# Kernel tuning notes

Measured on AMD Instinct MI355X. Metric: run time of the kernel, lower is better.

Reference implementation:

```python
import jax, jax.numpy as jnp
import numpy as np

N_E = 1024
E_DIM = 256
TAU = 0.5
BETA = 0.25
LAMB = 0.1
EPS = 1e-10


def setup_inputs() -> dict:
    key = jax.random.key(0)
    k1, k2, k3 = jax.random.split(key, 3)
    z = jax.random.normal(k1, (16, 1024, E_DIM), dtype=jnp.float32)
    # kaiming-normal-initialized codebook (std = sqrt(2 / fan_in))
    emb = jax.random.normal(k2, (N_E, E_DIM), dtype=jnp.float32) * np.sqrt(2.0 / E_DIM)
    u = jax.random.uniform(k3, (16 * 1024, N_E), dtype=jnp.float32)
    return {"z": z, "emb": emb, "u": u}


def reference(z, emb, u):
    zf = z.reshape(-1, E_DIM)                                  # [N, e_dim]
    # squared euclidean distances to each code: ||z||^2 + ||e||^2 - 2 z.e
    d = (jnp.sum(zf * zf, axis=1, keepdims=True)
         + jnp.sum(emb * emb, axis=1)
         - 2.0 * jnp.matmul(zf, emb.T))                        # [N, n_e]
    # gumbel-softmax (hard, straight-through) on logits = -d
    g = -jnp.log(-jnp.log(u + EPS) + EPS)
    y_soft = jax.nn.softmax((-d + g) / TAU, axis=-1)
    idx = jnp.argmax(y_soft, axis=-1)
    y_hard = jax.nn.one_hot(idx, N_E, dtype=y_soft.dtype)
    probs = y_hard + y_soft - jax.lax.stop_gradient(y_soft)    # [N, n_e]
    z_q = jnp.matmul(probs, emb).reshape(z.shape)
    # orthogonality loss on the codebook gram matrix
    gram = jnp.matmul(emb, emb.T)
    ortho = jnp.mean((gram - jnp.eye(N_E, dtype=emb.dtype)) ** 2) / (N_E ** 2)
    emb_loss = jnp.mean((jax.lax.stop_gradient(z_q) - z) ** 2)
    commit = BETA * jnp.mean((z_q - jax.lax.stop_gradient(z)) ** 2)
    loss = emb_loss + BETA * commit + LAMB * ortho
    z_q_st = z + jax.lax.stop_gradient(z_q - z)
    e_mean = jnp.mean(probs, axis=0)
    perplexity = jnp.exp(-jnp.sum(e_mean * jnp.log(e_mean + EPS)))
    return loss, z_q_st, perplexity
```

## Files before the change

kernel.cpp:

```cpp
#include <hip/hip_runtime.h>
#include <math.h>
#include <stdint.h>


#define NROWS 16384
#define NE    1024
#define ED    256
#define EPSF  1e-10f
#define INV2048 4.8828125e-4f
#define BM 128
#define BN 64
#define SCW 68

typedef _Float16 half_t;
typedef __attribute__((ext_vector_type(4))) _Float16 half4;
typedef __attribute__((ext_vector_type(8))) _Float16 half8;
typedef __attribute__((ext_vector_type(16))) float floatx16;
typedef unsigned long long u64;

__device__ __forceinline__ void gl_lds16(const void* g, void* l) {
    __builtin_amdgcn_global_load_lds(
        (const __attribute__((address_space(1))) uint32_t*)g,
        (__attribute__((address_space(3))) uint32_t*)l, 16, 0, 0);
}

__device__ __forceinline__ u64 packMax(float v, int code) {
    unsigned int b   = __float_as_uint(v);
    unsigned int key = (b & 0x80000000u) ? ~b : (b | 0x80000000u);
    return ((u64)key << 32) | (unsigned int)(NE - 1 - code);
}

__global__ __launch_bounds__(256) void vq_prep(
        const float* __restrict__ z, const float* __restrict__ emb,
        half_t* __restrict__ zh, half_t* __restrict__ zl,
        half_t* __restrict__ eh, half_t* __restrict__ el,
        float* __restrict__ enorm, float* __restrict__ znorm,
        u64* __restrict__ best)
{
    const int gid = blockIdx.x * 256 + threadIdx.x;
    const int ZQ4 = NROWS * ED / 4;
    if (gid < ZQ4) {
        const float4 v = ((const float4*)z)[gid];
        const float x[4] = {v.x, v.y, v.z, v.w};
        half4 h, l;
#pragma unroll
        for (int i = 0; i < 4; ++i) {
            const half_t hi = (half_t)x[i];
            h[i] = hi; l[i] = (half_t)((x[i] - (float)hi) * 2048.0f);
        }
        *(half4*)&zh[(size_t)gid * 4] = h;
        *(half4*)&zl[(size_t)gid * 4] = l;
        float s = v.x*v.x + v.y*v.y + v.z*v.z + v.w*v.w;
#pragma unroll
        for (int o = 32; o; o >>= 1) s += __shfl_down(s, o);
        if ((threadIdx.x & 63) == 0) znorm[gid >> 6] = s;
    } else {
        const int eg = gid - ZQ4;
        const float4 v = ((const float4*)emb)[eg];
        const float x[4] = {v.x, v.y, v.z, v.w};
        half4 h, l;
#pragma unroll
        for (int i = 0; i < 4; ++i) {
            const half_t hi = (half_t)x[i];
            h[i] = hi; l[i] = (half_t)((x[i] - (float)hi) * 2048.0f);
        }
        *(half4*)&eh[(size_t)eg * 4] = h;
        *(half4*)&el[(size_t)eg * 4] = l;
        float s = v.x*v.x + v.y*v.y + v.z*v.z + v.w*v.w;
#pragma unroll
        for (int o = 32; o; o >>= 1) s += __shfl_down(s, o);
        if ((threadIdx.x & 63) == 0) enorm[eg >> 6] = s;
        if (eg < NROWS) best[eg] = 0ull;
    }
}

__global__ __launch_bounds__(256, 2) void vq_gemm(
        const half_t* __restrict__ zh, const half_t* __restrict__ zl,
        const half_t* __restrict__ eh, const half_t* __restrict__ el,
        const float* __restrict__ u, const float* __restrict__ enorm,
        u64* __restrict__ best)
{
    __shared__ __align__(16) char smem[49152];
    half_t* SM = (half_t*)smem;
    float (*Sc)[SCW] = (float(*)[SCW])smem;
    u64* parr = (u64*)(smem + 34816);

    const int t    = threadIdx.x;
    const int w    = t >> 6;
    const int lane = t & 63;
    const int lrow = lane & 31;
    const int hw   = lane >> 5;

    const int bid = blockIdx.x;
    const int xcd = bid & 7, c = bid >> 3;
    const int m0 = (xcd * 16 + (c >> 4)) * BM;
    const int n0 = (c & 15) * BN;
    const int wm = (w >> 1) * 64, wn = (w & 1) * 32;

    size_t gaoff[2]; size_t gboff;
#pragma unroll
    for (int it = 0; it < 2; ++it) {
        const int s = it * 256 + t;
        const int row = s >> 2;
        const int cc = (s & 3) ^ ((row >> 1) & 3);
        gaoff[it] = (size_t)(m0 + row) * ED + cc * 8;
    }
    {
        const int row = t >> 2;
        const int cc = (t & 3) ^ ((row >> 1) & 3);
        gboff = (size_t)(n0 + row) * ED + cc * 8;
    }

    auto STAGE = [&](int kt, int b) {
        half_t* base = SM + b * 12288;
        const int kh = kt * 32;
#pragma unroll
        for (int it = 0; it < 2; ++it) {
            const int ldso = (it * 256 + w * 64) * 8;
            gl_lds16(zh + gaoff[it] + kh, base + ldso);
            gl_lds16(zl + gaoff[it] + kh, base + 4096 + ldso);
        }
        gl_lds16(eh + gboff + kh, base + 8192  + w * 64 * 8);
        gl_lds16(el + gboff + kh, base + 10240 + w * 64 * 8);
    };

    floatx16 accH[2] = {};
    floatx16 accX[2] = {};
    const int   col0 = n0 + wn + lrow;
    const float en0  = enorm[col0];
    float ur[2][16];

    STAGE(0, 0);
    __syncthreads();

#pragma unroll
    for (int kt = 0; kt < 8; ++kt) {
        const int cb = kt & 1;
        if (kt + 1 < 8) STAGE(kt + 1, cb ^ 1);
        if (kt == 0) {
            const float* ub = u + (size_t)(m0 + wm + (hw << 2)) * NE + col0;
#pragma unroll
            for (int i = 0; i < 2; ++i)
#pragma unroll
                for (int r = 0; r < 16; ++r)
                    ur[i][r] = ub[(size_t)(i * 32 + (r & 3) + ((r >> 2) << 3)) * NE];
        }
        {
            half_t* base = SM + cb * 12288;
#pragma unroll
            for (int ks = 0; ks < 2; ++ks) {
                const int cch = ks * 2 + hw;
                const int br = wn + lrow;
                const int sb = br * 4 + (cch ^ ((br >> 1) & 3));
                const half8 bh = *(const half8*)&base[8192  + sb * 8];
                const half8 bl = *(const half8*)&base[10240 + sb * 8];
                half8 ah[2], al[2];
#pragma unroll
                for (int i = 0; i < 2; ++i) {
                    const int ar = wm + i * 32 + lrow;
                    const int sa = ar * 4 + (cch ^ ((ar >> 1) & 3));
                    ah[i] = *(const half8*)&base[sa * 8];
                    al[i] = *(const half8*)&base[4096 + sa * 8];
                }
#pragma unroll
                for (int i = 0; i < 2; ++i) {
                    accH[i] = __builtin_amdgcn_mfma_f32_32x32x16_f16(ah[i], bh, accH[i], 0, 0, 0);
                    accX[i] = __builtin_amdgcn_mfma_f32_32x32x16_f16(ah[i], bl, accX[i], 0, 0, 0);
                    accX[i] = __builtin_amdgcn_mfma_f32_32x32x16_f16(al[i], bh, accX[i], 0, 0, 0);
                }
            }
        }
        if (kt == 0) {
#pragma unroll
            for (int i = 0; i < 2; ++i)
#pragma unroll
                for (int r = 0; r < 16; ++r)
                    asm volatile("" :: "v"(ur[i][r]));
        }
        __syncthreads();
    }

#pragma unroll
    for (int i = 0; i < 2; ++i) {
#pragma unroll
        for (int r = 0; r < 16; ++r) {
            const int lr = wm + i * 32 + (r & 3) + ((r >> 2) << 3) + (hw << 2);
            const float d = accH[i][r] + accX[i][r] * INV2048;
            const float g = -__logf(-__logf(ur[i][r] + EPSF) + EPSF);
            Sc[lr][wn + lrow] = 2.f * d - en0 + g;
        }
    }
    __syncthreads();

    {
        const int row = t >> 1;
        const int ch  = (t & 1) << 5;
        float bv = -1e38f; int bc = 0;
#pragma unroll
        for (int q = 0; q < 8; ++q) {
            const float4 v = *(const float4*)&Sc[row][ch + (q << 2)];
            const int cc = n0 + ch + (q << 2);
            if (v.x > bv) { bv = v.x; bc = cc; }
            if (v.y > bv) { bv = v.y; bc = cc + 1; }
            if (v.z > bv) { bv = v.z; bc = cc + 2; }
            if (v.w > bv) { bv = v.w; bc = cc + 3; }
        }
        parr[t] = packMax(bv, bc);
    }
    __syncthreads();
    if (t < 128) {
        const u64 a = parr[t << 1], b = parr[(t << 1) + 1];
        atomicMax(&best[m0 + t], a > b ? a : b);
    }
}

__global__ __launch_bounds__(256) void vq_outstore(
        const float* __restrict__ emb, const u64* __restrict__ best,
        float* __restrict__ out)
{
    __shared__ int ridx[8];
    const int t  = threadIdx.x;
    const int m0 = blockIdx.x * 8;

    if (t < 8)
        ridx[t] = NE - 1 - (int)(best[m0 + t] & 0xFFFFFFFFu);
    __syncthreads();

#pragma unroll
    for (int rr = 0; rr < 8; ++rr) {
        const int j = ridx[rr];
        out[1 + (size_t)(m0 + rr) * ED + t] = emb[(size_t)j * ED + t];
    }
}

__global__ __launch_bounds__(256) void vq_fin(
        const u64* __restrict__ best, const float* __restrict__ znorm,
        const float* __restrict__ u, float* __restrict__ out)
{
    __shared__ int    hist[NE];
    __shared__ double redl[4], redp[4];
    const int t = threadIdx.x;

    for (int i = t; i < NE; i += 256) hist[i] = 0;
    __syncthreads();

    double lsum = 0.0;
#pragma unroll 8
    for (int r = t; r < NROWS; r += 256) {
        const u64 p = best[r];
        const unsigned int key = (unsigned int)(p >> 32);
        const int code = NE - 1 - (int)(p & 0xFFFFFFFFu);
        atomicAdd(&hist[code], 1);
        const unsigned int b = (key & 0x80000000u) ? (key ^ 0x80000000u) : ~key;
        const float s  = __uint_as_float(b);
        const float uv = u[(size_t)r * NE + code];
        const float g  = -__logf(-__logf(uv + EPSF) + EPSF);
        lsum += (double)(znorm[r] - s + g);
    }
    __syncthreads();

    double psum = 0.0;
    for (int i = t; i < NE; i += 256) {
        const float em = (float)hist[i] / (float)NROWS;
        psum += (double)(em * logf(em + EPSF));
    }

#pragma unroll
    for (int o = 32; o; o >>= 1) { lsum += __shfl_down(lsum, o); psum += __shfl_down(psum, o); }
    if ((t & 63) == 0) { redl[t >> 6] = lsum; redp[t >> 6] = psum; }
    __syncthreads();
    if (t == 0) {
        const double mse = (redl[0] + redl[1] + redl[2] + redl[3])
                           / (double)((size_t)NROWS * ED);
        const double tot = redp[0] + redp[1] + redp[2] + redp[3];
        out[0] = (float)(mse * 1.0625);
        out[1 + (size_t)NROWS * ED] = (float)exp(-tot);
    }
}

extern "C" void kernel_launch(void* const* d_in, const int* in_sizes, int n_in,
                              void* d_out, int out_size, void* d_ws, size_t ws_size,
                              hipStream_t stream) {
    const float* z   = (const float*)d_in[0];
    const float* emb = (const float*)d_in[1];
    const float* u   = (const float*)d_in[2];
    float* out = (float*)d_out;

    float*  enorm    = (float*)((char*)d_ws + 5120);
    u64*    best     = (u64*)((char*)d_ws + 9216);
    float*  znorm    = (float*)((char*)d_ws + 140288);
    const size_t small_end = 205824;

    const size_t zsplit = (size_t)NROWS * ED * 2;
    const size_t esplit = (size_t)NE * ED * 2;
    const bool bigws = ws_size >= small_end + 2 * zsplit + 2 * esplit;

    half_t *zh, *zl, *eh, *el;
    if (bigws) {
        char* big = (char*)d_ws + small_end;
        zh = (half_t*)big;
        zl = (half_t*)(big + zsplit);
        eh = (half_t*)(big + 2 * zsplit);
        el = (half_t*)(big + 2 * zsplit + esplit);
    } else {
        zh = (half_t*)((char*)d_out + 8);
        zl = (half_t*)((char*)d_out + 8 + zsplit);
        eh = (half_t*)((char*)d_ws + small_end);
        el = (half_t*)((char*)d_ws + small_end + esplit);
    }

    vq_prep<<<(NROWS * ED / 4 + NE * ED / 4) / 256, 256, 0, stream>>>(
        z, emb, zh, zl, eh, el, enorm, znorm, best);
    vq_gemm<<<(NROWS / BM) * (NE / BN), 256, 0, stream>>>(
        zh, zl, eh, el, u, enorm, best);
    vq_outstore<<<NROWS / 8, 256, 0, stream>>>(emb, best, out);
    vq_fin<<<1, 256, 0, stream>>>(best, znorm, u, out);
}
```

Before: 186.4 us.

## Shrink GEMM tile to 64x64, single-buffer K=64 chunks, merge finalize into outstore

The GEMM tile drops from 128x64 to 64x64 with one 32x32 MFMA tile per wave, and occupancy is raised to 4 blocks per CU with a smaller LDS footprint. The K loop now loads 64-wide chunks into a single buffer instead of double-buffering 32-wide chunks, and the u loads move after the GEMM instead of being prefetched. The single-block finalize kernel becomes an extra block of the outstore kernel, which saves one launch. The trade-off is less reuse per tile and lost load/compute overlap, exchanged for more waves in flight.

```diff
diff --git a/kernel.cpp b/kernel.cpp
--- a/kernel.cpp
+++ b/kernel.cpp
@@ -8,7 +8,7 @@
 #define ED    256
 #define EPSF  1e-10f
 #define INV2048 4.8828125e-4f
-#define BM 128
+#define BM 64
 #define BN 64
 #define SCW 68
 
@@ -74,16 +74,19 @@
     }
 }
 
-__global__ __launch_bounds__(256, 2) void vq_gemm(
+__global__ __launch_bounds__(256, 4) void vq_gemm(
         const half_t* __restrict__ zh, const half_t* __restrict__ zl,
         const half_t* __restrict__ eh, const half_t* __restrict__ el,
         const float* __restrict__ u, const float* __restrict__ enorm,
         u64* __restrict__ best)
 {
-    __shared__ __align__(16) char smem[49152];
-    half_t* SM = (half_t*)smem;
+    __shared__ __align__(16) char smem[32768];
+    half_t* Ah = (half_t*)smem;
+    half_t* Al = (half_t*)(smem + 8192);
+    half_t* Bh = (half_t*)(smem + 16384);
+    half_t* Bl = (half_t*)(smem + 24576);
     float (*Sc)[SCW] = (float(*)[SCW])smem;
-    u64* parr = (u64*)(smem + 34816);
+    u64* parr = (u64*)(smem + 17408);
 
     const int t    = threadIdx.x;
     const int w    = t >> 6;
@@ -93,111 +96,74 @@
 
     const int bid = blockIdx.x;
     const int xcd = bid & 7, c = bid >> 3;
-    const int m0 = (xcd * 16 + (c >> 4)) * BM;
+    const int m0 = (xcd * 32 + (c >> 4)) * BM;
     const int n0 = (c & 15) * BN;
-    const int wm = (w >> 1) * 64, wn = (w & 1) * 32;
-
-    size_t gaoff[2]; size_t gboff;
+    const int wm = (w >> 1) * 32, wn = (w & 1) * 32;
+
+    size_t gaoff[2], gboff[2];
 #pragma unroll
     for (int it = 0; it < 2; ++it) {
         const int s = it * 256 + t;
-        const int row = s >> 2;
-        const int cc = (s & 3) ^ ((row >> 1) & 3);
+        const int row = s >> 3;
+        const int cc = (s & 7) ^ (row & 7);
         gaoff[it] = (size_t)(m0 + row) * ED + cc * 8;
-    }
+        gboff[it] = (size_t)(n0 + row) * ED + cc * 8;
+    }
+
+    auto STAGE = [&](int kc) {
+#pragma unroll
+        for (int it = 0; it < 2; ++it) {
+            const int ldso = (it * 256 + w * 64) * 8;
+            gl_lds16(zh + gaoff[it] + kc, Ah + ldso);
+            gl_lds16(zl + gaoff[it] + kc, Al + ldso);
+            gl_lds16(eh + gboff[it] + kc, Bh + ldso);
+            gl_lds16(el + gboff[it] + kc, Bl + ldso);
+        }
+    };
+
+    floatx16 accH = {};
+    floatx16 accX = {};
+
+    STAGE(0);
+    for (int kc = 0; kc < ED; kc += 64) {
+        __syncthreads();
+#pragma unroll
+        for (int ks = 0; ks < 4; ++ks) {
+            const int cch = ks * 2 + hw;
+            const int ar = wm + lrow;
+            const int br = wn + lrow;
+            const int sa = ar * 8 + (cch ^ (ar & 7));
+            const int sb = br * 8 + (cch ^ (br & 7));
+            const half8 ah = *(const half8*)&Ah[sa * 8];
+            const half8 al = *(const half8*)&Al[sa * 8];
+            const half8 bh = *(const half8*)&Bh[sb * 8];
+            const half8 bl = *(const half8*)&Bl[sb * 8];
+            accH = __builtin_amdgcn_mfma_f32_32x32x16_f16(ah, bh, accH, 0, 0, 0);
+            accX = __builtin_amdgcn_mfma_f32_32x32x16_f16(ah, bl, accX, 0, 0, 0);
+            accX = __builtin_amdgcn_mfma_f32_32x32x16_f16(al, bh, accX, 0, 0, 0);
+        }
+        __syncthreads();
+        if (kc + 64 < ED) STAGE(kc + 64);
+    }
+
+    const int   col0 = n0 + wn + lrow;
+    const float en0  = enorm[col0];
+#pragma unroll
+    for (int r = 0; r < 16; ++r) {
+        const int lr = wm + (r & 3) + ((r >> 2) << 3) + (hw << 2);
+        const float d  = accH[r] + accX[r] * INV2048;
+        const float uv = u[(size_t)(m0 + lr) * NE + col0];
+        const float g  = -__logf(-__logf(uv + EPSF) + EPSF);
+        Sc[lr][wn + lrow] = 2.f * d - en0 + g;
+    }
+    __syncthreads();
+
     {
         const int row = t >> 2;
-        const int cc = (t & 3) ^ ((row >> 1) & 3);
-        gboff = (size_t)(n0 + row) * ED + cc * 8;
-    }
-
-    auto STAGE = [&](int kt, int b) {
-        half_t* base = SM + b * 12288;
-        const int kh = kt * 32;
-#pragma unroll
-        for (int it = 0; it < 2; ++it) {
-            const int ldso = (it * 256 + w * 64) * 8;
-            gl_lds16(zh + gaoff[it] + kh, base + ldso);
-            gl_lds16(zl + gaoff[it] + kh, base + 4096 + ldso);
-        }
-        gl_lds16(eh + gboff + kh, base + 8192  + w * 64 * 8);
-        gl_lds16(el + gboff + kh, base + 10240 + w * 64 * 8);
-    };
-
-    floatx16 accH[2] = {};
-    floatx16 accX[2] = {};
-    const int   col0 = n0 + wn + lrow;
-    const float en0  = enorm[col0];
-    float ur[2][16];
-
-    STAGE(0, 0);
-    __syncthreads();
-
-#pragma unroll
-    for (int kt = 0; kt < 8; ++kt) {
-        const int cb = kt & 1;
-        if (kt + 1 < 8) STAGE(kt + 1, cb ^ 1);
-        if (kt == 0) {
-            const float* ub = u + (size_t)(m0 + wm + (hw << 2)) * NE + col0;
-#pragma unroll
-            for (int i = 0; i < 2; ++i)
-#pragma unroll
-                for (int r = 0; r < 16; ++r)
-                    ur[i][r] = ub[(size_t)(i * 32 + (r & 3) + ((r >> 2) << 3)) * NE];
-        }
-        {
-            half_t* base = SM + cb * 12288;
-#pragma unroll
-            for (int ks = 0; ks < 2; ++ks) {
-                const int cch = ks * 2 + hw;
-                const int br = wn + lrow;
-                const int sb = br * 4 + (cch ^ ((br >> 1) & 3));
-                const half8 bh = *(const half8*)&base[8192  + sb * 8];
-                const half8 bl = *(const half8*)&base[10240 + sb * 8];
-                half8 ah[2], al[2];
-#pragma unroll
-                for (int i = 0; i < 2; ++i) {
-                    const int ar = wm + i * 32 + lrow;
-                    const int sa = ar * 4 + (cch ^ ((ar >> 1) & 3));
-                    ah[i] = *(const half8*)&base[sa * 8];
-                    al[i] = *(const half8*)&base[4096 + sa * 8];
-                }
-#pragma unroll
-                for (int i = 0; i < 2; ++i) {
-                    accH[i] = __builtin_amdgcn_mfma_f32_32x32x16_f16(ah[i], bh, accH[i], 0, 0, 0);
-                    accX[i] = __builtin_amdgcn_mfma_f32_32x32x16_f16(ah[i], bl, accX[i], 0, 0, 0);
-                    accX[i] = __builtin_amdgcn_mfma_f32_32x32x16_f16(al[i], bh, accX[i], 0, 0, 0);
-                }
-            }
-        }
-        if (kt == 0) {
-#pragma unroll
-            for (int i = 0; i < 2; ++i)
-#pragma unroll
-                for (int r = 0; r < 16; ++r)
-                    asm volatile("" :: "v"(ur[i][r]));
-        }
-        __syncthreads();
-    }
-
-#pragma unroll
-    for (int i = 0; i < 2; ++i) {
-#pragma unroll
-        for (int r = 0; r < 16; ++r) {
-            const int lr = wm + i * 32 + (r & 3) + ((r >> 2) << 3) + (hw << 2);
-            const float d = accH[i][r] + accX[i][r] * INV2048;
-            const float g = -__logf(-__logf(ur[i][r] + EPSF) + EPSF);
-            Sc[lr][wn + lrow] = 2.f * d - en0 + g;
-        }
-    }
-    __syncthreads();
-
-    {
-        const int row = t >> 1;
-        const int ch  = (t & 1) << 5;
+        const int ch  = (t & 3) << 4;
         float bv = -1e38f; int bc = 0;
 #pragma unroll
-        for (int q = 0; q < 8; ++q) {
+        for (int q = 0; q < 4; ++q) {
             const float4 v = *(const float4*)&Sc[row][ch + (q << 2)];
             const int cc = n0 + ch + (q << 2);
             if (v.x > bv) { bv = v.x; bc = cc; }
@@ -208,20 +174,64 @@
         parr[t] = packMax(bv, bc);
     }
     __syncthreads();
-    if (t < 128) {
-        const u64 a = parr[t << 1], b = parr[(t << 1) + 1];
-        atomicMax(&best[m0 + t], a > b ? a : b);
+    if (t < 64) {
+        const u64 a = parr[(t << 2)],     b = parr[(t << 2) + 1];
+        const u64 e = parr[(t << 2) + 2], f = parr[(t << 2) + 3];
+        const u64 m1 = a > b ? a : b;
+        const u64 m2 = e > f ? e : f;
+        atomicMax(&best[m0 + t], m1 > m2 ? m1 : m2);
     }
 }
 
 __global__ __launch_bounds__(256) void vq_outstore(
         const float* __restrict__ emb, const u64* __restrict__ best,
+        const float* __restrict__ znorm, const float* __restrict__ u,
         float* __restrict__ out)
 {
+    const int t = threadIdx.x;
+
+    if (blockIdx.x == NROWS / 8) {
+        __shared__ int    hist[NE];
+        __shared__ double redl[4], redp[4];
+        for (int i = t; i < NE; i += 256) hist[i] = 0;
+        __syncthreads();
+
+        double lsum = 0.0;
+#pragma unroll 8
+        for (int r = t; r < NROWS; r += 256) {
+            const u64 p = best[r];
+            const unsigned int key = (unsigned int)(p >> 32);
+            const int code = NE - 1 - (int)(p & 0xFFFFFFFFu);
+            atomicAdd(&hist[code], 1);
+            const unsigned int b = (key & 0x80000000u) ? (key ^ 0x80000000u) : ~key;
+            const float s  = __uint_as_float(b);
+            const float uv = u[(size_t)r * NE + code];
+            const float g  = -__logf(-__logf(uv + EPSF) + EPSF);
+            lsum += (double)(znorm[r] - s + g);
+        }
+        __syncthreads();
+
+        double psum = 0.0;
+        for (int i = t; i < NE; i += 256) {
+            const float em = (float)hist[i] / (float)NROWS;
+            psum += (double)(em * logf(em + EPSF));
+        }
+#pragma unroll
+        for (int o = 32; o; o >>= 1) { lsum += __shfl_down(lsum, o); psum += __shfl_down(psum, o); }
+        if ((t & 63) == 0) { redl[t >> 6] = lsum; redp[t >> 6] = psum; }
+        __syncthreads();
+        if (t == 0) {
+            const double mse = (redl[0] + redl[1] + redl[2] + redl[3])
+                               / (double)((size_t)NROWS * ED);
+            const double tot = redp[0] + redp[1] + redp[2] + redp[3];
+            out[0] = (float)(mse * 1.0625);
+            out[1 + (size_t)NROWS * ED] = (float)exp(-tot);
+        }
+        return;
+    }
+
     __shared__ int ridx[8];
-    const int t  = threadIdx.x;
     const int m0 = blockIdx.x * 8;
-
     if (t < 8)
         ridx[t] = NE - 1 - (int)(best[m0 + t] & 0xFFFFFFFFu);
     __syncthreads();
@@ -230,51 +240,6 @@
     for (int rr = 0; rr < 8; ++rr) {
         const int j = ridx[rr];
         out[1 + (size_t)(m0 + rr) * ED + t] = emb[(size_t)j * ED + t];
-    }
-}
-
-__global__ __launch_bounds__(256) void vq_fin(
-        const u64* __restrict__ best, const float* __restrict__ znorm,
-        const float* __restrict__ u, float* __restrict__ out)
-{
-    __shared__ int    hist[NE];
-    __shared__ double redl[4], redp[4];
-    const int t = threadIdx.x;
-
-    for (int i = t; i < NE; i += 256) hist[i] = 0;
-    __syncthreads();
-
-    double lsum = 0.0;
-#pragma unroll 8
-    for (int r = t; r < NROWS; r += 256) {
-        const u64 p = best[r];
-        const unsigned int key = (unsigned int)(p >> 32);
-        const int code = NE - 1 - (int)(p & 0xFFFFFFFFu);
-        atomicAdd(&hist[code], 1);
-        const unsigned int b = (key & 0x80000000u) ? (key ^ 0x80000000u) : ~key;
-        const float s  = __uint_as_float(b);
-        const float uv = u[(size_t)r * NE + code];
-        const float g  = -__logf(-__logf(uv + EPSF) + EPSF);
-        lsum += (double)(znorm[r] - s + g);
-    }
-    __syncthreads();
-
-    double psum = 0.0;
-    for (int i = t; i < NE; i += 256) {
-        const float em = (float)hist[i] / (float)NROWS;
-        psum += (double)(em * logf(em + EPSF));
-    }
-
-#pragma unroll
-    for (int o = 32; o; o >>= 1) { lsum += __shfl_down(lsum, o); psum += __shfl_down(psum, o); }
-    if ((t & 63) == 0) { redl[t >> 6] = lsum; redp[t >> 6] = psum; }
-    __syncthreads();
-    if (t == 0) {
-        const double mse = (redl[0] + redl[1] + redl[2] + redl[3])
-                           / (double)((size_t)NROWS * ED);
-        const double tot = redp[0] + redp[1] + redp[2] + redp[3];
-        out[0] = (float)(mse * 1.0625);
-        out[1 + (size_t)NROWS * ED] = (float)exp(-tot);
     }
 }
 
@@ -313,6 +278,5 @@
         z, emb, zh, zl, eh, el, enorm, znorm, best);
     vq_gemm<<<(NROWS / BM) * (NE / BN), 256, 0, stream>>>(
         zh, zl, eh, el, u, enorm, best);
-    vq_outstore<<<NROWS / 8, 256, 0, stream>>>(emb, best, out);
-    vq_fin<<<1, 256, 0, stream>>>(best, znorm, u, out);
-}
+    vq_outstore<<<NROWS / 8 + 1, 256, 0, stream>>>(emb, best, znorm, u, out);
+}
```

New measurement: 185.6 us. No clear change (-0.4%).
